# Kernel optimization log

Measured on AMD Instinct MI355X. Metric: run time of the kernel, lower is better.

Reference implementation:

```python
import jax, jax.numpy as jnp
import numpy as np

N, E = 30000, 480000
D_IN, D_HID = 128, 256
NODE_CLS, EDGE_CLS, POLAR = 5, 2, 6
EPS = 1e-5

def layer_norm(x, g, b):
    mu = jnp.mean(x, axis=-1, keepdims=True)
    var = jnp.mean((x - mu) ** 2, axis=-1, keepdims=True)
    return g * (x - mu) / jnp.sqrt(var + EPS) + b

def sage_pool(h, src, dst, Wp, bp, Ws, bs, Wn, n_nodes):
    # DGL SAGEConv aggregator_type='pool': m = relu(fc_pool(h_src)); max over in-edges
    m = jax.nn.relu(h @ Wp + bp)              # [N, d_in]
    agg = jax.ops.segment_max(m[src], dst, num_segments=n_nodes)  # [N, d_in], -inf if no in-edges
    deg = jax.ops.segment_sum(jnp.ones((src.shape[0],), jnp.float32), dst, num_segments=n_nodes)
    h_neigh = jnp.where(deg[:, None] > 0, agg, 0.0)
    out = h @ Ws + bs + h_neigh @ Wn          # fc_self + fc_neigh
    return jax.nn.relu(out)                   # activation=F.relu

def setup_inputs() -> dict:
    key = jax.random.key(0)
    ks = jax.random.split(key, 24)
    p = lambda k, shape, fan: jax.random.normal(k, shape, jnp.float32) / np.sqrt(fan)
    return {
        "h": jax.random.normal(ks[0], (N, D_IN), jnp.float32),
        "efeat": jax.random.normal(ks[1], (E, POLAR), jnp.float32),
        "src": jax.random.randint(ks[2], (E,), 0, N, jnp.int32),
        "dst": jax.random.randint(ks[3], (E,), 0, N, jnp.int32),
        # encoder SAGEConv(128->256)
        "enc_Wpool": p(ks[4], (D_IN, D_IN), D_IN), "enc_bpool": jnp.zeros((D_IN,), jnp.float32),
        "enc_Wself": p(ks[5], (D_IN, D_HID), D_IN), "enc_bself": jnp.zeros((D_HID,), jnp.float32),
        "enc_Wneigh": p(ks[6], (D_IN, D_HID), D_IN),
        # node_pred: Linear(256,5) + LayerNorm(5)
        "np_W": p(ks[7], (D_HID, NODE_CLS), D_HID), "np_b": jnp.zeros((NODE_CLS,), jnp.float32),
        "np_g": jnp.ones((NODE_CLS,), jnp.float32), "np_beta": jnp.zeros((NODE_CLS,), jnp.float32),
        # edge predictor: Linear(528,256) + LN(256) + Linear(256,2)
        "ep_W1": p(ks[8], (2 * D_HID + 2 * NODE_CLS + POLAR, D_HID), 2 * D_HID + 16),
        "ep_b1": jnp.zeros((D_HID,), jnp.float32),
        "ep_g": jnp.ones((D_HID,), jnp.float32), "ep_beta": jnp.zeros((D_HID,), jnp.float32),
        "ep_W2": p(ks[9], (D_HID, EDGE_CLS), D_HID), "ep_b2": jnp.zeros((EDGE_CLS,), jnp.float32),
        # decoder SAGEConv(256->128)
        "dec_Wpool": p(ks[10], (D_HID, D_HID), D_HID), "dec_bpool": jnp.zeros((D_HID,), jnp.float32),
        "dec_Wself": p(ks[11], (D_HID, D_IN), D_HID), "dec_bself": jnp.zeros((D_IN,), jnp.float32),
        "dec_Wneigh": p(ks[12], (D_HID, D_IN), D_HID),
    }

def reference(h, efeat, src, dst,
              enc_Wpool, enc_bpool, enc_Wself, enc_bself, enc_Wneigh,
              np_W, np_b, np_g, np_beta,
              ep_W1, ep_b1, ep_g, ep_beta, ep_W2, ep_b2,
              dec_Wpool, dec_bpool, dec_Wself, dec_bself, dec_Wneigh):
    # encoder (drop_rate == 0 path)
    h1 = sage_pool(h, src, dst, enc_Wpool, enc_bpool, enc_Wself, enc_bself, enc_Wneigh, N)
    # node head
    node_pred = layer_norm(h1 @ np_W + np_b, np_g, np_beta)  # [N, 5]
    # edge head: gather-concat-MLP per edge
    cls_sm = jax.nn.softmax(node_pred, axis=1)               # softmax once, gather per edge
    x = jnp.concatenate([h1[src], cls_sm[src], efeat, h1[dst], cls_sm[dst]], axis=1)  # [E, 528]
    x = jax.nn.relu(layer_norm(x @ ep_W1 + ep_b1, ep_g, ep_beta))
    edges_pred = x @ ep_W2 + ep_b2                           # dropout is identity in eval
    # decoder (uses original graph, input h1)
    h2 = sage_pool(h1, src, dst, dec_Wpool, dec_bpool, dec_Wself, dec_bself, dec_Wneigh, N)
    return (node_pred, edges_pred, h2)
```

## Files before the change

kernel.cpp:

```cpp
#include <hip/hip_runtime.h>

typedef unsigned short u16;
typedef unsigned int u32;
typedef __bf16 bf16_t;
typedef bf16_t bf16x8 __attribute__((ext_vector_type(8)));
typedef float f32x4 __attribute__((ext_vector_type(4)));
typedef float f32x2 __attribute__((ext_vector_type(2)));

#define N_NODES 30000
#define N_EDGES 480000

static __device__ __forceinline__ float b2f(u16 u) {
  return __uint_as_float(((u32)u) << 16);
}
static __device__ __forceinline__ float b2f_lo(u32 w) {
  return __uint_as_float(w << 16);
}
static __device__ __forceinline__ float b2f_hi(u32 w) {
  return __uint_as_float(w & 0xffff0000u);
}
static __device__ __forceinline__ u16 f2b(float f) {
  u32 x = __float_as_uint(f);
  u32 r = (x + 0x7fffu + ((x >> 16) & 1u)) >> 16;
  return (u16)r;
}

__global__ __launch_bounds__(256) void init_sniff_deg(const u16* __restrict__ h,
                                                      int* __restrict__ flag,
                                                      int* __restrict__ deg) {
  int i = blockIdx.x * 256 + threadIdx.x;
  if (i < N_NODES) deg[i] = 0;
  if (blockIdx.x == 0) {
    int t = threadIdx.x;
    int bad = 0;
#pragma unroll
    for (int j = 0; j < 4; j++) {
      u32 e = ((u32)h[t * 4 + j] >> 7) & 0xFFu;
      if (e >= 0x8Eu) bad = 1;
    }
    int r = __syncthreads_or(bad);
    if (t == 0) *flag = r ? 1 : 0;
  }
}

struct ConvDesc { const void* s; u16* d; int n; int off; };
struct ConvTab { ConvDesc e[20]; int total; };

__global__ __launch_bounds__(256) void conv_all(
    const int* __restrict__ dstE, int* __restrict__ deg,
    const void* __restrict__ hsrc, u16* __restrict__ c_h,
    const void* __restrict__ efsrc, u16* __restrict__ c_ef,
    ConvTab tab, const int* __restrict__ flag) {
  int b = blockIdx.x;
  const int t = threadIdx.x;
  if (b < 1875) {
    int e = b * 256 + t;
    if (e < N_EDGES) atomicAdd(&deg[dstE[e]], 1);
    return;
  }
  b -= 1875;
  const int f = *flag;
  if (b < 3750) {
    int i = b * 256 + t;
    if (f) {
      float4 v = ((const float4*)hsrc)[i];
      uint2 o;
      o.x = (u32)f2b(v.x) | ((u32)f2b(v.y) << 16);
      o.y = (u32)f2b(v.z) | ((u32)f2b(v.w) << 16);
      ((uint2*)c_h)[i] = o;
    } else {
      ((uint2*)c_h)[i] = ((const uint2*)hsrc)[i];
    }
    return;
  }
  b -= 3750;
  if (b < 2813) {
    int i = b * 256 + t;
    if (i < 720000) {
      if (f) {
        float4 v = ((const float4*)efsrc)[i];
        uint2 o;
        o.x = (u32)f2b(v.x) | ((u32)f2b(v.y) << 16);
        o.y = (u32)f2b(v.z) | ((u32)f2b(v.w) << 16);
        ((uint2*)c_ef)[i] = o;
      } else {
        ((uint2*)c_ef)[i] = ((const uint2*)efsrc)[i];
      }
    }
    return;
  }
  b -= 2813;
  int i = b * 256 + t;
  if (i >= tab.total) return;
#pragma unroll 1
  for (int a = 0; a < 20; a++) {
    int j = i - tab.e[a].off;
    if (j >= 0 && j < tab.e[a].n) {
      if (f) tab.e[a].d[j] = f2b(((const float*)tab.e[a].s)[j]);
      else tab.e[a].d[j] = ((const u16*)tab.e[a].s)[j];
      return;
    }
  }
}

__global__ __launch_bounds__(1024) void scan_off(const int* __restrict__ deg,
                                                 int* __restrict__ off,
                                                 int* __restrict__ cursor, int n) {
  __shared__ int carry;
  __shared__ int wsum[16];
  int t = threadIdx.x, lane = t & 63, wv = t >> 6;
  if (t == 0) { carry = 0; off[0] = 0; }
  __syncthreads();
  for (int base = 0; base < n; base += 1024) {
    int v = (base + t < n) ? deg[base + t] : 0;
    int x = v;
#pragma unroll
    for (int d = 1; d < 64; d <<= 1) {
      int y = __shfl_up(x, d, 64);
      if (lane >= d) x += y;
    }
    if (lane == 63) wsum[wv] = x;
    __syncthreads();
    int wadd = 0;
    for (int w = 0; w < wv; w++) wadd += wsum[w];
    int incl = x + wadd + carry;
    if (base + t < n) { off[base + t + 1] = incl; cursor[base + t] = incl - v; }
    __syncthreads();
    if (t == 1023) carry = incl;
    __syncthreads();
  }
}

__global__ __launch_bounds__(256) void fill_csr(const int* __restrict__ src,
                                                const int* __restrict__ dst,
                                                int* __restrict__ cursor,
                                                int* __restrict__ esrc,
                                                int* __restrict__ epos, int nE) {
  int e = blockIdx.x * 256 + threadIdx.x;
  if (e >= nE) return;
  int p = atomicAdd(&cursor[dst[e]], 1);
  esrc[p] = src[e];
  epos[e] = p;
}

#define MRG(r)                                                    \
  do {                                                            \
    a0 = max(a0, (r).x & 0xffffu); a1 = max(a1, (r).x >> 16);     \
    a2 = max(a2, (r).y & 0xffffu); a3 = max(a3, (r).y >> 16);     \
    a4 = max(a4, (r).z & 0xffffu); a5 = max(a5, (r).z >> 16);     \
    a6 = max(a6, (r).w & 0xffffu); a7 = max(a7, (r).w >> 16);     \
  } while (0)

__global__ __launch_bounds__(256) void agg128(const u16* __restrict__ m,
                                              const int* __restrict__ esrc,
                                              const int* __restrict__ off,
                                              u16* __restrict__ out) {
  int wv = threadIdx.x >> 6, lane = threadIdx.x & 63;
  int qd = lane >> 4, l = lane & 15;
  int n = blockIdx.x * 16 + wv * 4 + qd;
  if (n >= N_NODES) return;
  int i = off[n], s1 = off[n + 1];
  u32 a0 = 0, a1 = 0, a2 = 0, a3 = 0, a4 = 0, a5 = 0, a6 = 0, a7 = 0;
  for (; i + 1 < s1; i += 2) {
    int e0 = esrc[i], e1 = esrc[i + 1];
    uint4 r0 = *(const uint4*)(m + (size_t)e0 * 128 + l * 8);
    uint4 r1 = *(const uint4*)(m + (size_t)e1 * 128 + l * 8);
    MRG(r0); MRG(r1);
  }
  if (i < s1) {
    uint4 r0 = *(const uint4*)(m + (size_t)esrc[i] * 128 + l * 8);
    MRG(r0);
  }
  uint4 w;
  w.x = a0 | (a1 << 16); w.y = a2 | (a3 << 16);
  w.z = a4 | (a5 << 16); w.w = a6 | (a7 << 16);
  *(uint4*)(out + (size_t)n * 128 + l * 8) = w;
}

__global__ __launch_bounds__(256) void agg256(const u16* __restrict__ m,
                                              const int* __restrict__ esrc,
                                              const int* __restrict__ off,
                                              u16* __restrict__ out) {
  int wv = threadIdx.x >> 6, lane = threadIdx.x & 63;
  int half = lane >> 5, l = lane & 31;
  int n = blockIdx.x * 8 + wv * 2 + half;
  if (n >= N_NODES) return;
  int i = off[n], s1 = off[n + 1];
  u32 a0 = 0, a1 = 0, a2 = 0, a3 = 0, a4 = 0, a5 = 0, a6 = 0, a7 = 0;
  for (; i + 1 < s1; i += 2) {
    int e0 = esrc[i], e1 = esrc[i + 1];
    uint4 r0 = *(const uint4*)(m + (size_t)e0 * 256 + l * 8);
    uint4 r1 = *(const uint4*)(m + (size_t)e1 * 256 + l * 8);
    MRG(r0); MRG(r1);
  }
  if (i < s1) {
    uint4 r0 = *(const uint4*)(m + (size_t)esrc[i] * 256 + l * 8);
    MRG(r0);
  }
  uint4 w;
  w.x = a0 | (a1 << 16); w.y = a2 | (a3 << 16);
  w.z = a4 | (a5 << 16); w.w = a6 | (a7 << 16);
  *(uint4*)(out + (size_t)n * 256 + l * 8) = w;
}
#undef MRG

__global__ __launch_bounds__(256) void prep_weights(
    const u16* __restrict__ encWp, const u16* __restrict__ encWs, const u16* __restrict__ encWn,
    const u16* __restrict__ decWp, const u16* __restrict__ decWs, const u16* __restrict__ decWn,
    const u16* __restrict__ epW1, const u16* __restrict__ epb1,
    u16* __restrict__ wt_encpool, u16* __restrict__ wt_enc,
    u16* __restrict__ wt_decpool, u16* __restrict__ wt_dec,
    u16* __restrict__ wt_UV, u16* __restrict__ b512, float* __restrict__ swsum) {
  int b = blockIdx.x;
  const int t = threadIdx.x;
  if (b < 64) {
    int idx = b * 256 + t; int k = idx >> 7, n = idx & 127;
    wt_encpool[n * 128 + k] = encWp[k * 128 + n]; return;
  }
  b -= 64;
  if (b < 128) {
    int idx = b * 256 + t; int k = idx >> 8, n = idx & 255;
    wt_enc[n * 256 + k] = encWs[k * 256 + n]; return;
  }
  b -= 128;
  if (b < 128) {
    int idx = b * 256 + t; int k = idx >> 8, n = idx & 255;
    wt_enc[n * 256 + 128 + k] = encWn[k * 256 + n]; return;
  }
  b -= 128;
  if (b < 256) {
    int idx = b * 256 + t; int k = idx >> 8, n = idx & 255;
    wt_decpool[n * 256 + k] = decWp[k * 256 + n]; return;
  }
  b -= 256;
  if (b < 128) {
    int idx = b * 256 + t; int k = idx >> 7, n = idx & 127;
    wt_dec[n * 512 + k] = decWs[k * 128 + n]; return;
  }
  b -= 128;
  if (b < 128) {
    int idx = b * 256 + t; int k = idx >> 7, n = idx & 127;
    wt_dec[n * 512 + 256 + k] = decWn[k * 128 + n]; return;
  }
  b -= 128;
  if (b < 512) {
    int n = b, n2 = n & 255, base = (n >= 256) ? 267 : 0;
    for (int kp = t; kp < 288; kp += 256) {
      u16 v = (kp < 261) ? epW1[(size_t)(base + kp) * 256 + n2] : (u16)0;
      wt_UV[(size_t)n * 288 + kp] = v;
    }
    return;
  }
  b -= 512;
  if (b < 2) {
    int i = b * 256 + t;
    b512[i] = (i < 256) ? epb1[i] : (u16)0; return;
  }
  int k = t >> 5, l32 = t & 31;
  if (k < 6) {
    uint4 v = *(const uint4*)(epW1 + (size_t)(261 + k) * 256 + l32 * 8);
    float s = b2f_lo(v.x) + b2f_hi(v.x) + b2f_lo(v.y) + b2f_hi(v.y) +
              b2f_lo(v.z) + b2f_hi(v.z) + b2f_lo(v.w) + b2f_hi(v.w);
#pragma unroll
    for (int m = 1; m < 32; m <<= 1) s += __shfl_xor(s, m, 64);
    if (l32 == 0) swsum[k] = s;
  }
}

__global__ __launch_bounds__(256) void gemm_mfma(
    const u16* __restrict__ A0, const u16* __restrict__ A1, int K0, int K1,
    const u16* __restrict__ Bt, const u16* __restrict__ bias, int do_relu,
    u16* __restrict__ C, float* __restrict__ Cf, const int* __restrict__ flag,
    int M, int Nld) {
  __shared__ __align__(16) u16 As[128 * 40];
  __shared__ __align__(16) u16 Bs[128 * 40];
  const int t = threadIdx.x;
  const int lane = t & 63, wv = t >> 6;
  const int wm = wv & 1, wn = wv >> 1;
  const int r = lane & 15, q = lane >> 4;
  const int bm = blockIdx.x, bn = blockIdx.y;
  const int Ktot = K0 + K1;
  const bool usef = (Cf != nullptr) && (*flag != 0);

  f32x4 acc[4][4];
#pragma unroll
  for (int i = 0; i < 4; i++)
#pragma unroll
    for (int j = 0; j < 4; j++) acc[i][j] = (f32x4){0.f, 0.f, 0.f, 0.f};

  for (int kc = 0; kc < Ktot; kc += 32) {
#pragma unroll
    for (int h = 0; h < 2; h++) {
      int idx = t + h * 256;
      int rr = idx >> 2, qq = idx & 3;
      int rowg = bm * 128 + rr;
      uint4 av = make_uint4(0, 0, 0, 0);
      if (rowg < M) {
        const u16* p = (kc < K0) ? (A0 + (size_t)rowg * K0 + kc)
                                 : (A1 + (size_t)rowg * K1 + (kc - K0));
        av = *(const uint4*)(p + qq * 8);
      }
      *(uint4*)&As[rr * 40 + qq * 8] = av;
      int ng = bn * 128 + rr;
      uint4 bv = *(const uint4*)(Bt + (size_t)ng * Ktot + kc + qq * 8);
      *(uint4*)&Bs[rr * 40 + qq * 8] = bv;
    }
    __syncthreads();
    bf16x8 af[4], bfm[4];
#pragma unroll
    for (int mi = 0; mi < 4; mi++)
      af[mi] = *(const bf16x8*)&As[(wm * 64 + mi * 16 + r) * 40 + q * 8];
#pragma unroll
    for (int ni = 0; ni < 4; ni++)
      bfm[ni] = *(const bf16x8*)&Bs[(wn * 64 + ni * 16 + r) * 40 + q * 8];
#pragma unroll
    for (int mi = 0; mi < 4; mi++)
#pragma unroll
      for (int ni = 0; ni < 4; ni++)
        acc[mi][ni] = __builtin_amdgcn_mfma_f32_16x16x32_bf16(af[mi], bfm[ni], acc[mi][ni], 0, 0, 0);
    __syncthreads();
  }

  float bv[4];
#pragma unroll
  for (int ni = 0; ni < 4; ni++)
    bv[ni] = bias ? b2f(bias[bn * 128 + wn * 64 + ni * 16 + r]) : 0.f;
#pragma unroll
  for (int mi = 0; mi < 4; mi++) {
#pragma unroll
    for (int i = 0; i < 4; i++) {
      int rowg = bm * 128 + wm * 64 + mi * 16 + q * 4 + i;
      if (rowg >= M) continue;
#pragma unroll
      for (int ni = 0; ni < 4; ni++) {
        int colg = bn * 128 + wn * 64 + ni * 16 + r;
        float v = acc[mi][ni][i] + bv[ni];
        if (do_relu) v = v > 0.f ? v : 0.f;
        if (usef) Cf[(size_t)rowg * Nld + colg] = v;
        else C[(size_t)rowg * Nld + colg] = f2b(v);
      }
    }
  }
}

__global__ __launch_bounds__(256) void node_head(
    const u16* __restrict__ h1, const u16* __restrict__ W, const u16* __restrict__ b,
    const u16* __restrict__ g, const u16* __restrict__ beta,
    u16* __restrict__ outN, float* __restrict__ outNf, const int* __restrict__ flag,
    u16* __restrict__ smOut) {
  __shared__ float Wl[256 * 5];
  __shared__ float bl[5], gl[5], betal[5];
  int t = threadIdx.x;
#pragma unroll
  for (int c = 0; c < 5; c++) Wl[t * 5 + c] = b2f(W[t * 5 + c]);
  if (t < 5) { bl[t] = b2f(b[t]); gl[t] = b2f(g[t]); betal[t] = b2f(beta[t]); }
  __syncthreads();
  int n = blockIdx.x * 256 + t;
  if (n >= N_NODES) return;
  const bool usef = (*flag != 0);
  float acc[5] = {0.f, 0.f, 0.f, 0.f, 0.f};
  const u16* hp = h1 + (size_t)n * 256;
  for (int k8 = 0; k8 < 32; k8++) {
    uint4 v = *(const uint4*)(hp + k8 * 8);
    u32 wds[4] = {v.x, v.y, v.z, v.w};
#pragma unroll
    for (int h = 0; h < 4; h++) {
      float x0 = b2f_lo(wds[h]), x1 = b2f_hi(wds[h]);
      int k = k8 * 8 + h * 2;
#pragma unroll
      for (int c = 0; c < 5; c++)
        acc[c] += x0 * Wl[k * 5 + c] + x1 * Wl[(k + 1) * 5 + c];
    }
  }
  float x[5], mu = 0.f;
#pragma unroll
  for (int c = 0; c < 5; c++) { x[c] = acc[c] + bl[c]; mu += x[c]; }
  mu *= 0.2f;
  float var = 0.f;
#pragma unroll
  for (int c = 0; c < 5; c++) { float d = x[c] - mu; var += d * d; }
  var *= 0.2f;
  float rstd = rsqrtf(fmaxf(var, 0.f) + 1e-5f);
  float v5[5], mx = -1e30f;
#pragma unroll
  for (int c = 0; c < 5; c++) {
    v5[c] = gl[c] * (x[c] - mu) * rstd + betal[c];
    if (usef) outNf[(size_t)n * 5 + c] = v5[c];
    else outN[(size_t)n * 5 + c] = f2b(v5[c]);
    mx = fmaxf(mx, v5[c]);
  }
  float s = 0.f, ex[5];
#pragma unroll
  for (int c = 0; c < 5; c++) { ex[c] = __expf(v5[c] - mx); s += ex[c]; }
  float inv = 1.f / s;
  u16 row[32];
#pragma unroll
  for (int c = 0; c < 5; c++) row[c] = f2b(ex[c] * inv);
#pragma unroll
  for (int c = 5; c < 32; c++) row[c] = 0;
#pragma unroll
  for (int c = 0; c < 4; c++)
    *(uint4*)(smOut + (size_t)n * 32 + c * 8) = *(const uint4*)&row[c * 8];
}

__global__ __launch_bounds__(256) void rowsum_uv(const u16* __restrict__ UV,
                                                 float2* __restrict__ Srow) {
  int wv = threadIdx.x >> 6, lane = threadIdx.x & 63;
  int n = blockIdx.x * 4 + wv;
  if (n >= N_NODES) return;
  uint4 v = *(const uint4*)(UV + (size_t)n * 512 + lane * 8);
  float s = b2f_lo(v.x) + b2f_hi(v.x) + b2f_lo(v.y) + b2f_hi(v.y) +
            b2f_lo(v.z) + b2f_hi(v.z) + b2f_lo(v.w) + b2f_hi(v.w);
#pragma unroll
  for (int m = 1; m < 32; m <<= 1) s += __shfl_xor(s, m, 64);
  if (lane == 0) Srow[n].x = s;
  if (lane == 32) Srow[n].y = s;
}

__global__ __launch_bounds__(256) void edge_mean(
    const int* __restrict__ src, const int* __restrict__ dst,
    const u16* __restrict__ ef, const float2* __restrict__ Srow,
    const float* __restrict__ swsum, const int* __restrict__ epos,
    uint4* __restrict__ recs) {
  int e = blockIdx.x * 256 + threadIdx.x;
  if (e >= N_EDGES) return;
  int s0 = src[e], d0 = dst[e];
  const u32* efp = (const u32*)(ef + (size_t)e * 6);
  u32 f0 = efp[0], f1 = efp[1], f2 = efp[2];
  float xa[6] = {b2f_lo(f0), b2f_hi(f0), b2f_lo(f1), b2f_hi(f1), b2f_lo(f2), b2f_hi(f2)};
  float sw[6];
#pragma unroll
  for (int k = 0; k < 6; k++) sw[k] = swsum[k];
  float m0 = Srow[s0].x + Srow[d0].y;
#pragma unroll
  for (int k = 0; k < 6; k++) m0 += xa[k] * sw[k];
  m0 *= (1.f / 256.f);
  int p = epos[e];
  uint4 r0, r1;
  r0.x = (u32)s0; r0.y = (u32)e; r0.z = __float_as_uint(m0); r0.w = f0;
  r1.x = f1; r1.y = f2; r1.z = 0; r1.w = 0;
  recs[(size_t)p * 2 + 0] = r0;
  recs[(size_t)p * 2 + 1] = r1;
}

__global__ __launch_bounds__(256) void edge_pt(
    const u16* __restrict__ UV, const uint4* __restrict__ recs,
    const int* __restrict__ off,
    const u16* __restrict__ w1raw,
    const u16* __restrict__ g, const u16* __restrict__ beta,
    const u16* __restrict__ w2, const u16* __restrict__ b2,
    u16* __restrict__ outE, float* __restrict__ outEf, const int* __restrict__ flag) {
  const int t = threadIdx.x;
  const int lane = t & 63;
  const int c0 = lane * 4;
  const int grp = (lane >> 4) & 3;
  f32x2 wefA[6], wefB[6];
#pragma unroll
  for (int k = 0; k < 6; k++) {
    u32 wa = *(const u32*)(w1raw + (size_t)(261 + k) * 256 + c0);
    u32 wb = *(const u32*)(w1raw + (size_t)(261 + k) * 256 + c0 + 2);
    wefA[k] = (f32x2){b2f_lo(wa), b2f_hi(wa)};
    wefB[k] = (f32x2){b2f_lo(wb), b2f_hi(wb)};
  }
  f32x2 glA = (f32x2){b2f(g[c0]), b2f(g[c0 + 1])};
  f32x2 glB = (f32x2){b2f(g[c0 + 2]), b2f(g[c0 + 3])};
  f32x2 blA = (f32x2){b2f(beta[c0]), b2f(beta[c0 + 1])};
  f32x2 blB = (f32x2){b2f(beta[c0 + 2]), b2f(beta[c0 + 3])};
  float w20[4], w21[4];
#pragma unroll
  for (int j = 0; j < 4; j++) {
    w20[j] = b2f(w2[(c0 + j) * 2]); w21[j] = b2f(w2[(c0 + j) * 2 + 1]);
  }
  const float b20 = b2f(b2[0]), b21 = b2f(b2[1]);
  const float bsel = (grp & 1) ? b21 : b20;
  const bool usef = (*flag != 0);
  const f32x2 zero2 = (f32x2){0.f, 0.f};

  const int n = __builtin_amdgcn_readfirstlane(blockIdx.x * 4 + (t >> 6));
  if (n >= N_NODES) return;
  int i = __builtin_amdgcn_readfirstlane(off[n]);
  const int s1 = __builtin_amdgcn_readfirstlane(off[n + 1]);
  if (i >= s1) return;
  uint2 vn = *(const uint2*)(UV + ((size_t)(u32)n << 9) + 256 + c0);
  const f32x2 vA = (f32x2){b2f_lo(vn.x), b2f_hi(vn.x)};
  const f32x2 vB = (f32x2){b2f_lo(vn.y), b2f_hi(vn.y)};

  for (; i < s1; i += 2) {
    const bool two = (i + 1 < s1);
    const int ib = two ? i + 1 : i;
    uint4 ra0 = recs[(size_t)i * 2], ra1 = recs[(size_t)i * 2 + 1];
    uint4 rb0 = recs[(size_t)ib * 2], rb1 = recs[(size_t)ib * 2 + 1];
    const int sa = (int)ra0.x, ea = (int)ra0.y;
    const int sb = (int)rb0.x, eb = (int)rb0.y;
    const float ma = __uint_as_float(ra0.z), mb = __uint_as_float(rb0.z);
    float xa[6] = {b2f_lo(ra0.w), b2f_hi(ra0.w), b2f_lo(ra1.x), b2f_hi(ra1.x),
                   b2f_lo(ra1.y), b2f_hi(ra1.y)};
    float xb[6] = {b2f_lo(rb0.w), b2f_hi(rb0.w), b2f_lo(rb1.x), b2f_hi(rb1.x),
                   b2f_lo(rb1.y), b2f_hi(rb1.y)};
    uint2 ua = *(const uint2*)(UV + ((size_t)(u32)sa << 9) + c0);
    uint2 ub = *(const uint2*)(UV + ((size_t)(u32)sb << 9) + c0);

    f32x2 yaA = (f32x2){b2f_lo(ua.x), b2f_hi(ua.x)} + vA;
    f32x2 yaB = (f32x2){b2f_lo(ua.y), b2f_hi(ua.y)} + vB;
    f32x2 ybA = (f32x2){b2f_lo(ub.x), b2f_hi(ub.x)} + vA;
    f32x2 ybB = (f32x2){b2f_lo(ub.y), b2f_hi(ub.y)} + vB;
#pragma unroll
    for (int k = 0; k < 6; k++) {
      yaA += xa[k] * wefA[k];
      yaB += xa[k] * wefB[k];
      ybA += xb[k] * wefA[k];
      ybB += xb[k] * wefB[k];
    }
    float pqa = yaA.x * yaA.x;
    pqa += yaA.y * yaA.y; pqa += yaB.x * yaB.x; pqa += yaB.y * yaB.y;
    float pqb = ybA.x * ybA.x;
    pqb += ybA.y * ybA.y; pqb += ybB.x * ybB.x; pqb += ybB.y * ybB.y;
    pqa += __shfl_xor(pqa, 32, 64);
    pqb += __shfl_xor(pqb, 32, 64);
    float z = (lane < 32) ? pqa : pqb;
#pragma unroll
    for (int m = 16; m >= 1; m >>= 1) z += __shfl_xor(z, m, 64);
    float zz = __shfl_xor(z, 32, 64);
    float pqa_t = (lane < 32) ? z : zz;
    float pqb_t = (lane < 32) ? zz : z;
    float rsa = rsqrtf(fmaxf(pqa_t * (1.f / 256.f) - ma * ma, 0.f) + 1e-5f);
    float rsb = rsqrtf(fmaxf(pqb_t * (1.f / 256.f) - mb * mb, 0.f) + 1e-5f);
    f32x2 nAa = __builtin_elementwise_max((yaA - ma) * rsa * glA + blA, zero2);
    f32x2 nAb = __builtin_elementwise_max((yaB - ma) * rsa * glB + blB, zero2);
    f32x2 nBa = __builtin_elementwise_max((ybA - mb) * rsb * glA + blA, zero2);
    f32x2 nBb = __builtin_elementwise_max((ybB - mb) * rsb * glB + blB, zero2);
    float p0a = nAa.x * w20[0], p1a = nAa.x * w21[0];
    p0a += nAa.y * w20[1]; p1a += nAa.y * w21[1];
    p0a += nAb.x * w20[2]; p1a += nAb.x * w21[2];
    p0a += nAb.y * w20[3]; p1a += nAb.y * w21[3];
    float p0b = nBa.x * w20[0], p1b = nBa.x * w21[0];
    p0b += nBa.y * w20[1]; p1b += nBa.y * w21[1];
    p0b += nBb.x * w20[2]; p1b += nBb.x * w21[2];
    p0b += nBb.y * w20[3]; p1b += nBb.y * w21[3];
    p0a += __shfl_xor(p0a, 32, 64); p1a += __shfl_xor(p1a, 32, 64);
    p0b += __shfl_xor(p0b, 32, 64); p1b += __shfl_xor(p1b, 32, 64);
    p0a += __shfl_xor(p0a, 16, 64); p1a += __shfl_xor(p1a, 16, 64);
    p0b += __shfl_xor(p0b, 16, 64); p1b += __shfl_xor(p1b, 16, 64);
    float w = (grp & 2) ? ((grp & 1) ? p1b : p0b) : ((grp & 1) ? p1a : p0a);
#pragma unroll
    for (int m = 8; m >= 1; m >>= 1) w += __shfl_xor(w, m, 64);
    if ((lane & 15) == 0) {
      float val = w + bsel;
      if (grp & 2) {
        if (two) {
          size_t oi = (size_t)eb * 2 + (grp & 1);
          if (usef) outEf[oi] = val; else outE[oi] = f2b(val);
        }
      } else {
        size_t oi = (size_t)ea * 2 + (grp & 1);
        if (usef) outEf[oi] = val; else outE[oi] = f2b(val);
      }
    }
  }
}

extern "C" void kernel_launch(void* const* d_in, const int* in_sizes, int n_in,
                              void* d_out, int out_size, void* d_ws, size_t ws_size,
                              hipStream_t stream) {
  char* wp = (char*)d_ws;
  auto alloc = [&](size_t bytes) -> char* {
    char* p = wp; wp += (bytes + 255) & ~(size_t)255; return p;
  };
  int* flag       = (int*)alloc(256);
  u16* c_h        = (u16*)alloc((size_t)N_NODES * 128 * 2);
  u16* c_ef       = (u16*)alloc((size_t)N_EDGES * 6 * 2);
  static const int pidx[20] = {4,5,6,7,8, 9,10,11,12, 13,14,15,16,17,18, 19,20,21,22,23};
  static const int pn[20]   = {16384,128,32768,256,32768, 1280,5,5,5,
                               135168,256,256,256,512,2, 65536,256,32768,128,32768};
  u16* cp[20];
  for (int a = 0; a < 20; a++) cp[a] = (u16*)alloc((size_t)pn[a] * 2);

  u16* wt_encpool = (u16*)alloc(128 * 128 * 2);
  u16* wt_enc     = (u16*)alloc(256 * 256 * 2);
  u16* wt_decpool = (u16*)alloc(256 * 256 * 2);
  u16* wt_dec     = (u16*)alloc(128 * 512 * 2);
  u16* wt_UV      = (u16*)alloc(512 * 288 * 2);
  u16* b512       = (u16*)alloc(512 * 2);
  float2* Srow    = (float2*)alloc((size_t)N_NODES * 8);
  float* swsum_b  = (float*)alloc(64);
  u16* m_buf      = (u16*)alloc((size_t)N_NODES * 256 * 2);
  u16* aggb       = (u16*)alloc((size_t)N_NODES * 256 * 2);
  u16* UVbuf      = m_buf;
  u16* h1b        = (u16*)alloc((size_t)N_NODES * 256 * 2);
  u16* smb32      = (u16*)alloc((size_t)N_NODES * 32 * 2);
  int* deg        = (int*)alloc((size_t)N_NODES * 4);
  int* off        = (int*)alloc((size_t)(N_NODES + 1) * 4);
  int* cursor     = (int*)alloc((size_t)N_NODES * 4);
  int* esrc       = (int*)alloc((size_t)N_EDGES * 4);
  int* epos       = (int*)alloc((size_t)N_EDGES * 4);
  uint4* recs     = (uint4*)alloc(((size_t)N_EDGES * 2 + 8) * 16);

  const int* src = (const int*)d_in[2];
  const int* dst = (const int*)d_in[3];

  u16* outN = (u16*)d_out;
  u16* outE = outN + (size_t)N_NODES * 5;
  u16* outH = outN + 1110000;
  float* outNf = (float*)d_out;
  float* outEf = outNf + (size_t)N_NODES * 5;
  float* outHf = outNf + 1110000;

  init_sniff_deg<<<118, 256, 0, stream>>>((const u16*)d_in[0], flag, deg);
  ConvTab tab;
  int off_a = 0;
  for (int a = 0; a < 20; a++) {
    tab.e[a].s = d_in[pidx[a]]; tab.e[a].d = cp[a]; tab.e[a].n = pn[a]; tab.e[a].off = off_a;
    off_a += pn[a];
  }
  tab.total = off_a;
  int conv_blocks = 1875 + 3750 + 2813 + (off_a + 255) / 256;
  conv_all<<<conv_blocks, 256, 0, stream>>>(dst, deg, d_in[0], c_h, d_in[1], c_ef, tab, flag);

  const u16 *enc_Wpool = cp[0], *enc_bpool = cp[1], *enc_Wself = cp[2], *enc_bself = cp[3],
            *enc_Wneigh = cp[4], *np_W = cp[5], *np_b = cp[6], *np_g = cp[7], *np_beta = cp[8],
            *ep_W1 = cp[9], *ep_b1 = cp[10], *ep_g = cp[11], *ep_beta = cp[12],
            *ep_W2 = cp[13], *ep_b2 = cp[14], *dec_Wpool = cp[15], *dec_bpool = cp[16],
            *dec_Wself = cp[17], *dec_bself = cp[18], *dec_Wneigh = cp[19];

  scan_off<<<1, 1024, 0, stream>>>(deg, off, cursor, N_NODES);
  fill_csr<<<1875, 256, 0, stream>>>(src, dst, cursor, esrc, epos, N_EDGES);

  prep_weights<<<1347, 256, 0, stream>>>(enc_Wpool, enc_Wself, enc_Wneigh,
                                         dec_Wpool, dec_Wself, dec_Wneigh,
                                         ep_W1, ep_b1,
                                         wt_encpool, wt_enc, wt_decpool, wt_dec,
                                         wt_UV, b512, swsum_b);

  gemm_mfma<<<dim3(235, 1), 256, 0, stream>>>(c_h, nullptr, 128, 0, wt_encpool,
                                              enc_bpool, 1, m_buf, nullptr, flag, N_NODES, 128);
  agg128<<<1875, 256, 0, stream>>>(m_buf, esrc, off, aggb);
  gemm_mfma<<<dim3(235, 2), 256, 0, stream>>>(c_h, aggb, 128, 128, wt_enc,
                                              enc_bself, 1, h1b, nullptr, flag, N_NODES, 256);
  node_head<<<118, 256, 0, stream>>>(h1b, np_W, np_b, np_g, np_beta, outN, outNf, flag, smb32);
  gemm_mfma<<<dim3(235, 4), 256, 0, stream>>>(h1b, smb32, 256, 32, wt_UV,
                                              b512, 0, UVbuf, nullptr, flag, N_NODES, 512);
  rowsum_uv<<<7500, 256, 0, stream>>>(UVbuf, Srow);
  edge_mean<<<1875, 256, 0, stream>>>(src, dst, c_ef, Srow, swsum_b, epos, recs);
  edge_pt<<<7500, 256, 0, stream>>>(UVbuf, recs, off, ep_W1, ep_g, ep_beta, ep_W2, ep_b2,
                                    outE, outEf, flag);
  gemm_mfma<<<dim3(235, 2), 256, 0, stream>>>(h1b, nullptr, 256, 0, wt_decpool,
                                              dec_bpool, 1, m_buf, nullptr, flag, N_NODES, 256);
  agg256<<<3750, 256, 0, stream>>>(m_buf, esrc, off, aggb);
  gemm_mfma<<<dim3(235, 1), 256, 0, stream>>>(h1b, aggb, 256, 256, wt_dec,
                                              dec_bself, 1, outH, outHf, flag, N_NODES, 128);
}
```

Before: 477.2 us.

## Split edge MLP into fixed 32-edge chunks per wave instead of per-node

The edge predictor kernel now gives each wave a fixed run of 32 dst-sorted edge records instead of one destination node's whole in-edge list. The dst index is stored in each record so its V row can be gathered per edge, and the next record pair is prefetched one iteration ahead. This removes the load imbalance from varying node degree and the idle half-iteration on odd degrees. The cost is an extra V-row gather per edge, which should mostly hit cache since neighbouring records share a dst. The record buffer is padded and zeroed so the prefetch past the last edge reads valid memory.

```diff
diff --git a/kernel.cpp b/kernel.cpp
--- a/kernel.cpp
+++ b/kernel.cpp
@@ -423,7 +423,14 @@
     const float* __restrict__ swsum, const int* __restrict__ epos,
     uint4* __restrict__ recs) {
   int e = blockIdx.x * 256 + threadIdx.x;
-  if (e >= N_EDGES) return;
+  if (e >= N_EDGES) {
+    if (e < N_EDGES + 32) {
+      uint4 z = make_uint4(0, 0, 0, 0);
+      recs[(size_t)e * 2 + 0] = z;
+      recs[(size_t)e * 2 + 1] = z;
+    }
+    return;
+  }
   int s0 = src[e], d0 = dst[e];
   const u32* efp = (const u32*)(ef + (size_t)e * 6);
   u32 f0 = efp[0], f1 = efp[1], f2 = efp[2];
@@ -438,20 +445,19 @@
   int p = epos[e];
   uint4 r0, r1;
   r0.x = (u32)s0; r0.y = (u32)e; r0.z = __float_as_uint(m0); r0.w = f0;
-  r1.x = f1; r1.y = f2; r1.z = 0; r1.w = 0;
+  r1.x = f1; r1.y = f2; r1.z = (u32)d0; r1.w = 0;
   recs[(size_t)p * 2 + 0] = r0;
   recs[(size_t)p * 2 + 1] = r1;
 }
 
 __global__ __launch_bounds__(256) void edge_pt(
     const u16* __restrict__ UV, const uint4* __restrict__ recs,
-    const int* __restrict__ off,
     const u16* __restrict__ w1raw,
     const u16* __restrict__ g, const u16* __restrict__ beta,
     const u16* __restrict__ w2, const u16* __restrict__ b2,
     u16* __restrict__ outE, float* __restrict__ outEf, const int* __restrict__ flag) {
   const int t = threadIdx.x;
-  const int lane = t & 63;
+  const int lane = t & 63, wv = t >> 6;
   const int c0 = lane * 4;
   const int grp = (lane >> 4) & 3;
   f32x2 wefA[6], wefB[6];
@@ -476,34 +482,30 @@
   const bool usef = (*flag != 0);
   const f32x2 zero2 = (f32x2){0.f, 0.f};
 
-  const int n = __builtin_amdgcn_readfirstlane(blockIdx.x * 4 + (t >> 6));
-  if (n >= N_NODES) return;
-  int i = __builtin_amdgcn_readfirstlane(off[n]);
-  const int s1 = __builtin_amdgcn_readfirstlane(off[n + 1]);
-  if (i >= s1) return;
-  uint2 vn = *(const uint2*)(UV + ((size_t)(u32)n << 9) + 256 + c0);
-  const f32x2 vA = (f32x2){b2f_lo(vn.x), b2f_hi(vn.x)};
-  const f32x2 vB = (f32x2){b2f_lo(vn.y), b2f_hi(vn.y)};
-
-  for (; i < s1; i += 2) {
-    const bool two = (i + 1 < s1);
-    const int ib = two ? i + 1 : i;
-    uint4 ra0 = recs[(size_t)i * 2], ra1 = recs[(size_t)i * 2 + 1];
-    uint4 rb0 = recs[(size_t)ib * 2], rb1 = recs[(size_t)ib * 2 + 1];
-    const int sa = (int)ra0.x, ea = (int)ra0.y;
-    const int sb = (int)rb0.x, eb = (int)rb0.y;
-    const float ma = __uint_as_float(ra0.z), mb = __uint_as_float(rb0.z);
-    float xa[6] = {b2f_lo(ra0.w), b2f_hi(ra0.w), b2f_lo(ra1.x), b2f_hi(ra1.x),
-                   b2f_lo(ra1.y), b2f_hi(ra1.y)};
-    float xb[6] = {b2f_lo(rb0.w), b2f_hi(rb0.w), b2f_lo(rb1.x), b2f_hi(rb1.x),
-                   b2f_lo(rb1.y), b2f_hi(rb1.y)};
+  const int pb = __builtin_amdgcn_readfirstlane((blockIdx.x * 4 + wv) * 16);
+  const uint4* rp = recs + (size_t)pb * 4;
+  uint4 ra0 = rp[0], ra1 = rp[1], rb0 = rp[2], rb1 = rp[3];
+#pragma unroll 1
+  for (int it = 0; it < 16; ++it) {
+    uint4 ca0 = ra0, ca1 = ra1, cb0 = rb0, cb1 = rb1;
+    ra0 = rp[4 * it + 4]; ra1 = rp[4 * it + 5];
+    rb0 = rp[4 * it + 6]; rb1 = rp[4 * it + 7];
+    const int sa = (int)ca0.x, ea = (int)ca0.y, da = (int)ca1.z;
+    const int sb = (int)cb0.x, eb = (int)cb0.y, db = (int)cb1.z;
+    const float ma = __uint_as_float(ca0.z), mb = __uint_as_float(cb0.z);
+    float xa[6] = {b2f_lo(ca0.w), b2f_hi(ca0.w), b2f_lo(ca1.x), b2f_hi(ca1.x),
+                   b2f_lo(ca1.y), b2f_hi(ca1.y)};
+    float xb[6] = {b2f_lo(cb0.w), b2f_hi(cb0.w), b2f_lo(cb1.x), b2f_hi(cb1.x),
+                   b2f_lo(cb1.y), b2f_hi(cb1.y)};
     uint2 ua = *(const uint2*)(UV + ((size_t)(u32)sa << 9) + c0);
+    uint2 va = *(const uint2*)(UV + ((size_t)(u32)da << 9) + 256 + c0);
     uint2 ub = *(const uint2*)(UV + ((size_t)(u32)sb << 9) + c0);
-
-    f32x2 yaA = (f32x2){b2f_lo(ua.x), b2f_hi(ua.x)} + vA;
-    f32x2 yaB = (f32x2){b2f_lo(ua.y), b2f_hi(ua.y)} + vB;
-    f32x2 ybA = (f32x2){b2f_lo(ub.x), b2f_hi(ub.x)} + vA;
-    f32x2 ybB = (f32x2){b2f_lo(ub.y), b2f_hi(ub.y)} + vB;
+    uint2 vb = *(const uint2*)(UV + ((size_t)(u32)db << 9) + 256 + c0);
+
+    f32x2 yaA = (f32x2){b2f_lo(ua.x), b2f_hi(ua.x)} + (f32x2){b2f_lo(va.x), b2f_hi(va.x)};
+    f32x2 yaB = (f32x2){b2f_lo(ua.y), b2f_hi(ua.y)} + (f32x2){b2f_lo(va.y), b2f_hi(va.y)};
+    f32x2 ybA = (f32x2){b2f_lo(ub.x), b2f_hi(ub.x)} + (f32x2){b2f_lo(vb.x), b2f_hi(vb.x)};
+    f32x2 ybB = (f32x2){b2f_lo(ub.y), b2f_hi(ub.y)} + (f32x2){b2f_lo(vb.y), b2f_hi(vb.y)};
 #pragma unroll
     for (int k = 0; k < 6; k++) {
       yaA += xa[k] * wefA[k];
@@ -546,15 +548,9 @@
     for (int m = 8; m >= 1; m >>= 1) w += __shfl_xor(w, m, 64);
     if ((lane & 15) == 0) {
       float val = w + bsel;
-      if (grp & 2) {
-        if (two) {
-          size_t oi = (size_t)eb * 2 + (grp & 1);
-          if (usef) outEf[oi] = val; else outE[oi] = f2b(val);
-        }
-      } else {
-        size_t oi = (size_t)ea * 2 + (grp & 1);
-        if (usef) outEf[oi] = val; else outE[oi] = f2b(val);
-      }
+      size_t oi = (grp & 2) ? ((size_t)eb * 2 + (grp & 1)) : ((size_t)ea * 2 + (grp & 1));
+      if (usef) outEf[oi] = val;
+      else outE[oi] = f2b(val);
     }
   }
 }
@@ -593,7 +589,7 @@
   int* cursor     = (int*)alloc((size_t)N_NODES * 4);
   int* esrc       = (int*)alloc((size_t)N_EDGES * 4);
   int* epos       = (int*)alloc((size_t)N_EDGES * 4);
-  uint4* recs     = (uint4*)alloc(((size_t)N_EDGES * 2 + 8) * 16);
+  uint4* recs     = (uint4*)alloc(((size_t)(N_EDGES + 32) * 2) * 16);
 
   const int* src = (const int*)d_in[2];
   const int* dst = (const int*)d_in[3];
@@ -640,8 +636,8 @@
   gemm_mfma<<<dim3(235, 4), 256, 0, stream>>>(h1b, smb32, 256, 32, wt_UV,
                                               b512, 0, UVbuf, nullptr, flag, N_NODES, 512);
   rowsum_uv<<<7500, 256, 0, stream>>>(UVbuf, Srow);
-  edge_mean<<<1875, 256, 0, stream>>>(src, dst, c_ef, Srow, swsum_b, epos, recs);
-  edge_pt<<<7500, 256, 0, stream>>>(UVbuf, recs, off, ep_W1, ep_g, ep_beta, ep_W2, ep_b2,
+  edge_mean<<<1876, 256, 0, stream>>>(src, dst, c_ef, Srow, swsum_b, epos, recs);
+  edge_pt<<<3750, 256, 0, stream>>>(UVbuf, recs, ep_W1, ep_g, ep_beta, ep_W2, ep_b2,
                                     outE, outEf, flag);
   gemm_mfma<<<dim3(235, 2), 256, 0, stream>>>(h1b, nullptr, 256, 0, wt_decpool,
                                               dec_bpool, 1, m_buf, nullptr, flag, N_NODES, 256);
```

After: 471.2 us. Within noise of the previous version (-1.3%).
